# Kernel tuning notes

Measured on AMD Instinct MI355X. Metric: run time of the kernel, lower is better.

## Reference

```python
import jax, jax.numpy as jnp
import numpy as np

B, S, R, H = 32, 512, 196, 1024


def setup_inputs() -> dict:
    key = jax.random.key(0)
    ks = jax.random.split(key, 12)
    sc = 1.0 / np.sqrt(H)
    return {
        "dns_feature": jax.random.normal(ks[0], (B, S, H), jnp.float32),
        "img_features": jax.random.normal(ks[1], (B, R, H), jnp.float32),
        # attention 1 params (dns_linear_1 has bias, img_linear_1 does not)
        "W_d1": jax.random.normal(ks[2], (H, H), jnp.float32) * sc,
        "b_d1": jax.random.normal(ks[3], (H,), jnp.float32) * sc,
        "W_i1": jax.random.normal(ks[4], (H, H), jnp.float32) * sc,
        "w_att1": jax.random.normal(ks[5], (2 * H,), jnp.float32) * sc,
        "b_att1": jax.random.normal(ks[6], (), jnp.float32) * sc,
        # attention 2 params (img_linear_2 has bias, dns_linear_2 does not)
        "W_d2": jax.random.normal(ks[7], (H, H), jnp.float32) * sc,
        "W_i2": jax.random.normal(ks[8], (H, H), jnp.float32) * sc,
        "b_i2": jax.random.normal(ks[9], (H,), jnp.float32) * sc,
        "w_att2": jax.random.normal(ks[10], (2 * H,), jnp.float32) * sc,
        "b_att2": jax.random.normal(ks[11], (), jnp.float32) * sc,
    }


def reference(dns_feature, img_features, W_d1, b_d1, W_i1, w_att1, b_att1,
              W_d2, W_i2, b_i2, w_att2, b_att2):
    h = dns_feature.shape[-1]
    # --- attention 1: dns attends over image regions ---
    # original: tanh(concat(Lin(dns_rep), Lin(img_rep))) -> att_linear_1.
    # tanh is elementwise and the concat linear is separable, so
    # score[b,s,r] = wA . tanh(W_d1 dns[b,s] + b_d1) + wB . tanh(W_i1 img[b,r]) + b_att1
    dns_p = jnp.tanh(jnp.einsum('bsh,oh->bso', dns_feature, W_d1) + b_d1)   # (B,S,H)
    img_p = jnp.tanh(jnp.einsum('brh,oh->bro', img_features, W_i1))          # (B,R,H)
    wA, wB = w_att1[:h], w_att1[h:]
    scores1 = (jnp.einsum('bsh,h->bs', dns_p, wA)[:, :, None]
               + jnp.einsum('brh,h->br', img_p, wB)[:, None, :] + b_att1)    # (B,S,R)
    visual_att = jax.nn.softmax(scores1, axis=-1)
    att_img_features = jnp.einsum('bsr,brh->bsh', visual_att, img_features)  # (B,S,H)
    # --- attention 2: attended image (per token i) attends over dns tokens j ---
    # concat order is [img_proj, dns_proj] here.
    img_p2 = jnp.tanh(jnp.einsum('bih,oh->bio', att_img_features, W_i2) + b_i2)  # (B,S,H)
    dns_p2 = jnp.tanh(jnp.einsum('bjh,oh->bjo', dns_feature, W_d2))              # (B,S,H)
    wI, wD = w_att2[:h], w_att2[h:]
    scores2 = (jnp.einsum('bih,h->bi', img_p2, wI)[:, :, None]
               + jnp.einsum('bjh,h->bj', dns_p2, wD)[:, None, :] + b_att2)       # (B,S,S)
    textual_att = jax.nn.softmax(scores2, axis=-1)
    att_dns_features = jnp.einsum('bij,bjh->bih', textual_att, dns_feature)      # (B,S,H)
    return att_dns_features, att_img_features
```

## Files before the change

### kernel.cpp

```cpp
#include <hip/hip_runtime.h>
#include <hip/hip_bf16.h>
#include <stdint.h>

typedef __bf16 bh;
typedef __bf16 bf16x8 __attribute__((ext_vector_type(8)));
typedef float f32x4 __attribute__((ext_vector_type(4)));

#define B_  32
#define S_  512
#define R_  196
#define H_  1024
#define BH  (B_ * H_)


__device__ __forceinline__ float fast_tanh(float x) {
  x = fminf(10.f, fmaxf(-10.f, x));
  float e = __expf(2.f * x);
  return (e - 1.f) / (e + 1.f);
}

__device__ __forceinline__ bf16x8 cvt8(const float4 a, const float4 b) {
  bf16x8 r;
  r[0] = (bh)a.x; r[1] = (bh)a.y; r[2] = (bh)a.z; r[3] = (bh)a.w;
  r[4] = (bh)b.x; r[5] = (bh)b.y; r[6] = (bh)b.z; r[7] = (bh)b.w;
  return r;
}

__device__ __forceinline__ void gload_lds16(const bh* g, bh* l) {
  __builtin_amdgcn_global_load_lds(
      (__attribute__((address_space(1))) void*)g,
      (__attribute__((address_space(3))) void*)l,
      16, 0, 0);
}

#define G_DNS 2097152
#define G_IMG 802816
#define G_W   131072
#define G_TOT (G_DNS + G_IMG + 2 * G_W)

__global__ __launch_bounds__(256)
void convert_kernel(const float* __restrict__ dns, const float* __restrict__ img,
                    const float* __restrict__ Wd2, const float* __restrict__ Wi1,
                    bh* __restrict__ dnsB, bh* __restrict__ imgB,
                    bh* __restrict__ wd2B, bh* __restrict__ wi1B) {
  for (int g = blockIdx.x * 256 + threadIdx.x; g < G_TOT; g += gridDim.x * 256) {
    const float* src; bh* dst; int off;
    if (g < G_DNS)                    { src = dns; dst = dnsB; off = g; }
    else if (g < G_DNS + G_IMG)       { src = img; dst = imgB; off = g - G_DNS; }
    else if (g < G_DNS + G_IMG + G_W) { src = Wd2; dst = wd2B; off = g - G_DNS - G_IMG; }
    else                              { src = Wi1; dst = wi1B; off = g - G_DNS - G_IMG - G_W; }
    float4 a = ((const float4*)src)[(size_t)off * 2];
    float4 b = ((const float4*)src)[(size_t)off * 2 + 1];
    ((bf16x8*)dst)[off] = cvt8(a, b);
  }
}


__global__ __launch_bounds__(256, 3)
void score_gemm_kernel(const bh* __restrict__ dnsB, const bh* __restrict__ imgB,
                       const bh* __restrict__ Wd2B, const bh* __restrict__ Wi1B,
                       const float* __restrict__ watt1, const float* __restrict__ watt2,
                       float* __restrict__ sPartD, float* __restrict__ sPartB) {
  __shared__ __align__(16) bh As[2][128 * 32];
  __shared__ __align__(16) bh Bs[2][128 * 32];
  __shared__ float sred[128];

  const int tid = threadIdx.x;
  const int wave = tid >> 6, lane = tid & 63;

  const int d = blockIdx.x;
  const int k = (d & 7) * 177 + (d >> 3);
  const int my = k >> 3, ny = k & 7;

  const bh* X; const bh* W; const float* w; float* sp; int m0;
  if (my < 128) { X = dnsB; W = Wd2B; w = watt2 + H_; sp = sPartD; m0 = my * 128; }
  else          { X = imgB; W = Wi1B; w = watt1 + H_; sp = sPartB; m0 = (my - 128) * 128; }
  const int n0 = ny * 128;

  const int srow  = wave * 32 + (lane >> 2);
  const int ssege = (((lane & 3) ^ ((lane >> 2) & 2)) * 8);
  const bh* Ag = X + ((size_t)(m0 + srow) * H_ + ssege);
  const bh* Bg = W + ((size_t)(n0 + srow) * H_ + ssege);
  const int lw = wave * 32 * 32;

  const int wm = wave >> 1, wn = wave & 1;
  const int col = lane & 15, quad = lane >> 4;
  const int qx8 = ((quad ^ (col & 2)) * 8);

  f32x4 acc[4][4] = {};

  {
    gload_lds16(Ag,            &As[0][lw]);
    gload_lds16(Ag + 16 * H_,  &As[0][lw + 16 * 32]);
    gload_lds16(Bg,            &Bs[0][lw]);
    gload_lds16(Bg + 16 * H_,  &Bs[0][lw + 16 * 32]);
  }
  __syncthreads();

  for (int kt = 0; kt < 32; ++kt) {
    const int cur = kt & 1;
    if (kt + 1 < 32) {
      const int ko = (kt + 1) * 32;
      gload_lds16(Ag + ko,            &As[cur ^ 1][lw]);
      gload_lds16(Ag + ko + 16 * H_,  &As[cur ^ 1][lw + 16 * 32]);
      gload_lds16(Bg + ko,            &Bs[cur ^ 1][lw]);
      gload_lds16(Bg + ko + 16 * H_,  &Bs[cur ^ 1][lw + 16 * 32]);
    }

    bf16x8 af[4], bfr[4];
#pragma unroll
    for (int mi = 0; mi < 4; ++mi)
      af[mi] = *(const bf16x8*)(&As[cur][(wm * 64 + mi * 16 + col) * 32 + qx8]);
#pragma unroll
    for (int ni = 0; ni < 4; ++ni)
      bfr[ni] = *(const bf16x8*)(&Bs[cur][(wn * 64 + ni * 16 + col) * 32 + qx8]);

#pragma unroll
    for (int mi = 0; mi < 4; ++mi)
#pragma unroll
      for (int ni = 0; ni < 4; ++ni)
        acc[mi][ni] = __builtin_amdgcn_mfma_f32_16x16x32_bf16(af[mi], bfr[ni], acc[mi][ni], 0, 0, 0);

    __syncthreads();
  }

  float wv[4];
#pragma unroll
  for (int ni = 0; ni < 4; ++ni) wv[ni] = w[n0 + wn * 64 + ni * 16 + col];

  float ppv[4][4];
#pragma unroll
  for (int mi = 0; mi < 4; ++mi) {
#pragma unroll
    for (int reg = 0; reg < 4; ++reg) {
      float pp = 0.f;
#pragma unroll
      for (int ni = 0; ni < 4; ++ni) pp += fast_tanh(acc[mi][ni][reg]) * wv[ni];
      pp += __shfl_xor(pp, 1);
      pp += __shfl_xor(pp, 2);
      pp += __shfl_xor(pp, 4);
      pp += __shfl_xor(pp, 8);
      ppv[mi][reg] = pp;
    }
  }

  if (wn == 0 && col == 0) {
#pragma unroll
    for (int mi = 0; mi < 4; ++mi)
#pragma unroll
      for (int reg = 0; reg < 4; ++reg)
        sred[wm * 64 + mi * 16 + quad * 4 + reg] = ppv[mi][reg];
  }
  __syncthreads();
  if (wn == 1 && col == 0) {
#pragma unroll
    for (int mi = 0; mi < 4; ++mi)
#pragma unroll
      for (int reg = 0; reg < 4; ++reg) {
        int ml = wm * 64 + mi * 16 + quad * 4 + reg;
        sp[(size_t)(m0 + ml) * 8 + ny] = sred[ml] + ppv[mi][reg];
      }
  }
}

__global__ __launch_bounds__(256)
void wsum_kernel(const float* __restrict__ dns, const float* __restrict__ img,
                 const float* __restrict__ sPartD, const float* __restrict__ sPartB,
                 float* __restrict__ uPart, float* __restrict__ vPart) {
  __shared__ float red[4];
  __shared__ float es[512];
  const int b = blockIdx.x, tid = threadIdx.x, zc = blockIdx.y;
  const int wave = tid >> 6, lane = tid & 63;
  const int h = tid * 4;

  if (zc < 16) {
    const float4* p4 = (const float4*)(sPartD + (size_t)b * S_ * 8);
    float4 a0 = p4[tid * 2],        a1 = p4[tid * 2 + 1];
    float4 c0 = p4[(tid + 256) * 2], c1 = p4[(tid + 256) * 2 + 1];
    float x0 = a0.x + a0.y + a0.z + a0.w + a1.x + a1.y + a1.z + a1.w;
    float x1 = c0.x + c0.y + c0.z + c0.w + c1.x + c1.y + c1.z + c1.w;
    float m = fmaxf(x0, x1);
#pragma unroll
    for (int msk = 32; msk; msk >>= 1) m = fmaxf(m, __shfl_xor(m, msk));
    if (!lane) red[wave] = m;
    __syncthreads();
    float bm = fmaxf(fmaxf(red[0], red[1]), fmaxf(red[2], red[3]));
    __syncthreads();
    float e0 = __expf(x0 - bm), e1 = __expf(x1 - bm);
    es[tid] = e0; es[tid + 256] = e1;
    float s = e0 + e1;
#pragma unroll
    for (int msk = 32; msk; msk >>= 1) s += __shfl_xor(s, msk);
    if (!lane) red[wave] = s;
    __syncthreads();
    const float inv = 1.f / (red[0] + red[1] + red[2] + red[3]);

    const int j0 = zc * 32;
    const float* Xb = dns + ((size_t)(b * S_ + j0) * H_ + h);
    float4 a = {0.f, 0.f, 0.f, 0.f};
#pragma unroll
    for (int jj = 0; jj < 32; ++jj) {
      float4 xv = *(const float4*)(Xb + (size_t)jj * H_);
      float qv = es[j0 + jj] * inv;
      a.x += qv * xv.x; a.y += qv * xv.y; a.z += qv * xv.z; a.w += qv * xv.w;
    }
    *(float4*)(uPart + (size_t)zc * BH + (size_t)b * H_ + h) = a;
  } else {
    const float4* p4 = (const float4*)(sPartB + (size_t)b * R_ * 8);
    float x = -3.0e38f;
    if (tid < R_) {
      float4 a0 = p4[tid * 2], a1 = p4[tid * 2 + 1];
      x = a0.x + a0.y + a0.z + a0.w + a1.x + a1.y + a1.z + a1.w;
    }
    float m = x;
#pragma unroll
    for (int msk = 32; msk; msk >>= 1) m = fmaxf(m, __shfl_xor(m, msk));
    if (!lane) red[wave] = m;
    __syncthreads();
    float bm = fmaxf(fmaxf(red[0], red[1]), fmaxf(red[2], red[3]));
    __syncthreads();
    float e = (tid < R_) ? __expf(x - bm) : 0.f;
    es[tid] = e;
    float s = e;
#pragma unroll
    for (int msk = 32; msk; msk >>= 1) s += __shfl_xor(s, msk);
    if (!lane) red[wave] = s;
    __syncthreads();
    const float inv = 1.f / (red[0] + red[1] + red[2] + red[3]);

    const int j0 = (zc - 16) * 49;
    const float* Xb = img + ((size_t)(b * R_ + j0) * H_ + h);
    float4 a = {0.f, 0.f, 0.f, 0.f};
#pragma unroll
    for (int jj = 0; jj < 49; ++jj) {
      float4 xv = *(const float4*)(Xb + (size_t)jj * H_);
      float qv = es[j0 + jj] * inv;
      a.x += qv * xv.x; a.y += qv * xv.y; a.z += qv * xv.z; a.w += qv * xv.w;
    }
    *(float4*)(vPart + (size_t)(zc - 16) * BH + (size_t)b * H_ + h) = a;
  }
}

__global__ __launch_bounds__(256)
void bcast_kernel(const float* __restrict__ uPart, const float* __restrict__ vPart,
                  float* __restrict__ out) {
  const int id = blockIdx.x;
  const int b = id >> 4, sc = id & 15;
  const int t = threadIdx.x;

  float4 u4 = {0.f, 0.f, 0.f, 0.f};
#pragma unroll
  for (int c = 0; c < 16; ++c) {
    float4 s = ((const float4*)(uPart + (size_t)c * BH + (size_t)b * H_))[t];
    u4.x += s.x; u4.y += s.y; u4.z += s.z; u4.w += s.w;
  }
  float4 v4 = {0.f, 0.f, 0.f, 0.f};
#pragma unroll
  for (int c = 0; c < 4; ++c) {
    float4 s = ((const float4*)(vPart + (size_t)c * BH + (size_t)b * H_))[t];
    v4.x += s.x; v4.y += s.y; v4.z += s.z; v4.w += s.w;
  }

  const int PER4 = B_ * S_ * H_ / 4;
  float4* o0 = (float4*)out + ((size_t)(b * S_ + sc * 32)) * 256 + t;
  float4* o1 = o0 + PER4;
#pragma unroll
  for (int s = 0; s < 32; ++s) { o0[(size_t)s * 256] = u4; o1[(size_t)s * 256] = v4; }
}


extern "C" void kernel_launch(void* const* d_in, const int* in_sizes, int n_in,
                              void* d_out, int out_size, void* d_ws, size_t ws_size,
                              hipStream_t stream) {
  const float* dns   = (const float*)d_in[0];
  const float* img   = (const float*)d_in[1];
  const float* Wi1   = (const float*)d_in[4];
  const float* watt1 = (const float*)d_in[5];
  const float* Wd2   = (const float*)d_in[7];
  const float* watt2 = (const float*)d_in[10];
  float* out = (float*)d_out;

  float* ws = (float*)d_ws;
  float* sPartD = ws;
  float* sPartB = ws + 131072;
  float* uPart  = ws + 181248;
  float* vPart  = ws + 705536;
  bh* dnsB = (bh*)(ws + 836608);
  bh* imgB = (bh*)(ws + 9225216);
  bh* wd2B = (bh*)(ws + 12436480);
  bh* wi1B = (bh*)(ws + 12960768);

  convert_kernel<<<2048, 256, 0, stream>>>(dns, img, Wd2, Wi1, dnsB, imgB, wd2B, wi1B);
  score_gemm_kernel<<<1416, 256, 0, stream>>>(
      dnsB, imgB, wd2B, wi1B, watt1, watt2, sPartD, sPartB);
  wsum_kernel<<<dim3(B_, 20), 256, 0, stream>>>(dns, img, sPartD, sPartB, uPart, vPart);
  bcast_kernel<<<512, 256, 0, stream>>>(uPart, vPart, out);
}
```

Baseline: 323.9 us.

## Fuse weighted-sum and broadcast kernels, widen LDS swizzle, raise GEMM occupancy hint

Merges the softmax-weighted-sum and broadcast kernels into one kernel. Each block now computes both softmaxes, reduces a 64-wide H slice over all tokens and regions, and writes that slice to every output row, so the uPart/vPart partials no longer go through global memory and one launch is dropped. The score GEMM's LDS XOR swizzle now spreads over four segments instead of two to cut bank conflicts, and its launch bound goes from 3 to 4 blocks per SM, which may limit registers. The fused kernel launches only 512 blocks, and each block reads its full dns and img rows strided across H, which may lower memory parallelism.

Result: no change. 323.5 us (-0.1%).

```diff
diff --git a/kernel.cpp b/kernel.cpp
--- a/kernel.cpp
+++ b/kernel.cpp
@@ -56,7 +56,7 @@
 }
 
 
-__global__ __launch_bounds__(256, 3)
+__global__ __launch_bounds__(256, 4)
 void score_gemm_kernel(const bh* __restrict__ dnsB, const bh* __restrict__ imgB,
                        const bh* __restrict__ Wd2B, const bh* __restrict__ Wi1B,
                        const float* __restrict__ watt1, const float* __restrict__ watt2,
@@ -78,23 +78,21 @@
   const int n0 = ny * 128;
 
   const int srow  = wave * 32 + (lane >> 2);
-  const int ssege = (((lane & 3) ^ ((lane >> 2) & 2)) * 8);
+  const int ssege = (((lane & 3) ^ ((lane >> 3) & 3)) * 8);
   const bh* Ag = X + ((size_t)(m0 + srow) * H_ + ssege);
   const bh* Bg = W + ((size_t)(n0 + srow) * H_ + ssege);
   const int lw = wave * 32 * 32;
 
   const int wm = wave >> 1, wn = wave & 1;
   const int col = lane & 15, quad = lane >> 4;
-  const int qx8 = ((quad ^ (col & 2)) * 8);
+  const int qx8 = ((quad ^ ((col >> 1) & 3)) * 8);
 
   f32x4 acc[4][4] = {};
 
-  {
-    gload_lds16(Ag,            &As[0][lw]);
-    gload_lds16(Ag + 16 * H_,  &As[0][lw + 16 * 32]);
-    gload_lds16(Bg,            &Bs[0][lw]);
-    gload_lds16(Bg + 16 * H_,  &Bs[0][lw + 16 * 32]);
-  }
+  gload_lds16(Ag,            &As[0][lw]);
+  gload_lds16(Ag + 16 * H_,  &As[0][lw + 16 * 32]);
+  gload_lds16(Bg,            &Bs[0][lw]);
+  gload_lds16(Bg + 16 * H_,  &Bs[0][lw + 16 * 32]);
   __syncthreads();
 
   for (int kt = 0; kt < 32; ++kt) {
@@ -164,18 +162,23 @@
 }
 
 __global__ __launch_bounds__(256)
-void wsum_kernel(const float* __restrict__ dns, const float* __restrict__ img,
-                 const float* __restrict__ sPartD, const float* __restrict__ sPartB,
-                 float* __restrict__ uPart, float* __restrict__ vPart) {
+void wsum_bcast_kernel(const float* __restrict__ dns, const float* __restrict__ img,
+                       const float* __restrict__ sPartD, const float* __restrict__ sPartB,
+                       float* __restrict__ out) {
   __shared__ float red[4];
-  __shared__ float es[512];
-  const int b = blockIdx.x, tid = threadIdx.x, zc = blockIdx.y;
-  const int wave = tid >> 6, lane = tid & 63;
-  const int h = tid * 4;
-
-  if (zc < 16) {
+  __shared__ float esd[512];
+  __shared__ float esi[196];
+  __shared__ float4 aru[4][16];
+  __shared__ float4 arv[4][16];
+  __shared__ float4 su[16], sv[16];
+
+  const int b = blockIdx.x, hc = blockIdx.y;
+  const int tid = threadIdx.x, wave = tid >> 6, lane = tid & 63;
+  float inv_d, inv_i;
+
+  {
     const float4* p4 = (const float4*)(sPartD + (size_t)b * S_ * 8);
-    float4 a0 = p4[tid * 2],        a1 = p4[tid * 2 + 1];
+    float4 a0 = p4[tid * 2],         a1 = p4[tid * 2 + 1];
     float4 c0 = p4[(tid + 256) * 2], c1 = p4[(tid + 256) * 2 + 1];
     float x0 = a0.x + a0.y + a0.z + a0.w + a1.x + a1.y + a1.z + a1.w;
     float x1 = c0.x + c0.y + c0.z + c0.w + c1.x + c1.y + c1.z + c1.w;
@@ -187,28 +190,19 @@
     float bm = fmaxf(fmaxf(red[0], red[1]), fmaxf(red[2], red[3]));
     __syncthreads();
     float e0 = __expf(x0 - bm), e1 = __expf(x1 - bm);
-    es[tid] = e0; es[tid + 256] = e1;
+    esd[tid] = e0; esd[tid + 256] = e1;
     float s = e0 + e1;
 #pragma unroll
     for (int msk = 32; msk; msk >>= 1) s += __shfl_xor(s, msk);
     if (!lane) red[wave] = s;
     __syncthreads();
-    const float inv = 1.f / (red[0] + red[1] + red[2] + red[3]);
-
-    const int j0 = zc * 32;
-    const float* Xb = dns + ((size_t)(b * S_ + j0) * H_ + h);
-    float4 a = {0.f, 0.f, 0.f, 0.f};
-#pragma unroll
-    for (int jj = 0; jj < 32; ++jj) {
-      float4 xv = *(const float4*)(Xb + (size_t)jj * H_);
-      float qv = es[j0 + jj] * inv;
-      a.x += qv * xv.x; a.y += qv * xv.y; a.z += qv * xv.z; a.w += qv * xv.w;
-    }
-    *(float4*)(uPart + (size_t)zc * BH + (size_t)b * H_ + h) = a;
-  } else {
-    const float4* p4 = (const float4*)(sPartB + (size_t)b * R_ * 8);
+    inv_d = 1.f / (red[0] + red[1] + red[2] + red[3]);
+    __syncthreads();
+  }
+  {
     float x = -3.0e38f;
     if (tid < R_) {
+      const float4* p4 = (const float4*)(sPartB + (size_t)b * R_ * 8);
       float4 a0 = p4[tid * 2], a1 = p4[tid * 2 + 1];
       x = a0.x + a0.y + a0.z + a0.w + a1.x + a1.y + a1.z + a1.w;
     }
@@ -220,52 +214,72 @@
     float bm = fmaxf(fmaxf(red[0], red[1]), fmaxf(red[2], red[3]));
     __syncthreads();
     float e = (tid < R_) ? __expf(x - bm) : 0.f;
-    es[tid] = e;
+    if (tid < R_) esi[tid] = e;
     float s = e;
 #pragma unroll
     for (int msk = 32; msk; msk >>= 1) s += __shfl_xor(s, msk);
     if (!lane) red[wave] = s;
     __syncthreads();
-    const float inv = 1.f / (red[0] + red[1] + red[2] + red[3]);
-
-    const int j0 = (zc - 16) * 49;
-    const float* Xb = img + ((size_t)(b * R_ + j0) * H_ + h);
-    float4 a = {0.f, 0.f, 0.f, 0.f};
-#pragma unroll
-    for (int jj = 0; jj < 49; ++jj) {
-      float4 xv = *(const float4*)(Xb + (size_t)jj * H_);
-      float qv = es[j0 + jj] * inv;
-      a.x += qv * xv.x; a.y += qv * xv.y; a.z += qv * xv.z; a.w += qv * xv.w;
+    inv_i = 1.f / (red[0] + red[1] + red[2] + red[3]);
+    __syncthreads();
+  }
+
+  const int h4 = tid & 15, jg = tid >> 4;
+  const float* db = dns + (size_t)b * S_ * H_ + hc * 64 + h4 * 4;
+  float4 ua = {0.f, 0.f, 0.f, 0.f};
+#pragma unroll
+  for (int it = 0; it < 32; ++it) {
+    const int j = jg + it * 16;
+    float4 xv = *(const float4*)(db + (size_t)j * H_);
+    float qv = esd[j];
+    ua.x += qv * xv.x; ua.y += qv * xv.y; ua.z += qv * xv.z; ua.w += qv * xv.w;
+  }
+  const float* ib = img + (size_t)b * R_ * H_ + hc * 64 + h4 * 4;
+  float4 va = {0.f, 0.f, 0.f, 0.f};
+#pragma unroll
+  for (int it = 0; it < 13; ++it) {
+    const int j = jg + it * 16;
+    if (j < R_) {
+      float4 xv = *(const float4*)(ib + (size_t)j * H_);
+      float pv = esi[j];
+      va.x += pv * xv.x; va.y += pv * xv.y; va.z += pv * xv.z; va.w += pv * xv.w;
     }
-    *(float4*)(vPart + (size_t)(zc - 16) * BH + (size_t)b * H_ + h) = a;
-  }
-}
-
-__global__ __launch_bounds__(256)
-void bcast_kernel(const float* __restrict__ uPart, const float* __restrict__ vPart,
-                  float* __restrict__ out) {
-  const int id = blockIdx.x;
-  const int b = id >> 4, sc = id & 15;
-  const int t = threadIdx.x;
-
-  float4 u4 = {0.f, 0.f, 0.f, 0.f};
-#pragma unroll
-  for (int c = 0; c < 16; ++c) {
-    float4 s = ((const float4*)(uPart + (size_t)c * BH + (size_t)b * H_))[t];
-    u4.x += s.x; u4.y += s.y; u4.z += s.z; u4.w += s.w;
-  }
-  float4 v4 = {0.f, 0.f, 0.f, 0.f};
-#pragma unroll
-  for (int c = 0; c < 4; ++c) {
-    float4 s = ((const float4*)(vPart + (size_t)c * BH + (size_t)b * H_))[t];
-    v4.x += s.x; v4.y += s.y; v4.z += s.z; v4.w += s.w;
-  }
+  }
+#pragma unroll
+  for (int msk = 16; msk <= 32; msk <<= 1) {
+    ua.x += __shfl_xor(ua.x, msk); ua.y += __shfl_xor(ua.y, msk);
+    ua.z += __shfl_xor(ua.z, msk); ua.w += __shfl_xor(ua.w, msk);
+    va.x += __shfl_xor(va.x, msk); va.y += __shfl_xor(va.y, msk);
+    va.z += __shfl_xor(va.z, msk); va.w += __shfl_xor(va.w, msk);
+  }
+  if (lane < 16) { aru[wave][lane] = ua; arv[wave][lane] = va; }
+  __syncthreads();
+  if (tid < 16) {
+    float4 s0 = aru[0][tid], s1 = aru[1][tid], s2 = aru[2][tid], s3 = aru[3][tid];
+    float4 r;
+    r.x = (s0.x + s1.x + s2.x + s3.x) * inv_d;
+    r.y = (s0.y + s1.y + s2.y + s3.y) * inv_d;
+    r.z = (s0.z + s1.z + s2.z + s3.z) * inv_d;
+    r.w = (s0.w + s1.w + s2.w + s3.w) * inv_d;
+    su[tid] = r;
+    s0 = arv[0][tid]; s1 = arv[1][tid]; s2 = arv[2][tid]; s3 = arv[3][tid];
+    r.x = (s0.x + s1.x + s2.x + s3.x) * inv_i;
+    r.y = (s0.y + s1.y + s2.y + s3.y) * inv_i;
+    r.z = (s0.z + s1.z + s2.z + s3.z) * inv_i;
+    r.w = (s0.w + s1.w + s2.w + s3.w) * inv_i;
+    sv[tid] = r;
+  }
+  __syncthreads();
 
   const int PER4 = B_ * S_ * H_ / 4;
-  float4* o0 = (float4*)out + ((size_t)(b * S_ + sc * 32)) * 256 + t;
+  const float4 u4 = su[h4], v4 = sv[h4];
+  float4* o0 = (float4*)out + ((size_t)b * S_ + jg) * 256 + hc * 16 + h4;
   float4* o1 = o0 + PER4;
 #pragma unroll
-  for (int s = 0; s < 32; ++s) { o0[(size_t)s * 256] = u4; o1[(size_t)s * 256] = v4; }
+  for (int s = 0; s < 32; ++s) {
+    o0[(size_t)s * 16 * 256] = u4;
+    o1[(size_t)s * 16 * 256] = v4;
+  }
 }
 
 
@@ -283,16 +297,13 @@
   float* ws = (float*)d_ws;
   float* sPartD = ws;
   float* sPartB = ws + 131072;
-  float* uPart  = ws + 181248;
-  float* vPart  = ws + 705536;
-  bh* dnsB = (bh*)(ws + 836608);
-  bh* imgB = (bh*)(ws + 9225216);
-  bh* wd2B = (bh*)(ws + 12436480);
-  bh* wi1B = (bh*)(ws + 12960768);
+  bh* dnsB = (bh*)(ws + 181248);
+  bh* imgB = (bh*)(ws + 8569856);
+  bh* wd2B = (bh*)(ws + 11781120);
+  bh* wi1B = (bh*)(ws + 12305408);
 
   convert_kernel<<<2048, 256, 0, stream>>>(dns, img, Wd2, Wi1, dnsB, imgB, wd2B, wi1B);
   score_gemm_kernel<<<1416, 256, 0, stream>>>(
       dnsB, imgB, wd2B, wi1B, watt1, watt2, sPartD, sPartB);
-  wsum_kernel<<<dim3(B_, 20), 256, 0, stream>>>(dns, img, sPartD, sPartB, uPart, vPart);
-  bcast_kernel<<<512, 256, 0, stream>>>(uPart, vPart, out);
-}
+  wsum_bcast_kernel<<<dim3(B_, 16), 256, 0, stream>>>(dns, img, sPartD, sPartB, out);
+}
```
